# Performance work log

Hardware: AMD Instinct MI355X
Metric: run time of the kernel (lower is better)

Reference implementation:

```python
import jax, jax.numpy as jnp
import numpy as np

# PGA G(3,0,1) blade layout: [1, e0,e1,e2,e3, e01,e02,e03,e12,e13,e23, e012,e013,e023,e123, e0123]
GRADE = jnp.array([0, 1, 1, 1, 1, 2, 2, 2, 2, 2, 2, 3, 3, 3, 3, 4])
# invariant inner product uses only blades not containing the degenerate e0
INNER_IDX = jnp.array([0, 2, 3, 4, 8, 9, 10, 14])

B, N, IN_MV, IN_S = 1, 1024, 16, 128
H, HID_MV, HID_S = 8, 4, 32
C_Z, OUT_MV, OUT_S = 128, 16, 128
ROPE_BASE = 4096.0


def equi_linear(mv, w5):
    # grade-wise equivariant channel mixing: w5 [out, in, 5] -> per-blade weight [out, in, 16]
    w16 = w5[:, :, GRADE]
    return jnp.einsum('...ib,oib->...ob', mv, w16)


def rope(x, base=ROPE_BASE):
    # rotary positional encoding along item axis 1; last dim must be even
    n, d = x.shape[1], x.shape[-1]
    half = d // 2
    freqs = base ** (-jnp.arange(half, dtype=x.dtype) / half)
    ang = jnp.arange(n, dtype=x.dtype)[:, None] * freqs  # [N, half]
    shp = (1, n) + (1,) * (x.ndim - 3) + (half,)
    cos, sin = jnp.cos(ang).reshape(shp), jnp.sin(ang).reshape(shp)
    x1, x2 = x[..., 0::2], x[..., 1::2]
    return jnp.stack([x1 * cos - x2 * sin, x1 * sin + x2 * cos], axis=-1).reshape(x.shape)


def setup_inputs() -> dict:
    key = jax.random.key(0)
    ks = jax.random.split(key, 16)
    sc_mv = 1.0 / np.sqrt(IN_MV)
    sc_s = 1.0 / np.sqrt(IN_S)
    return {
        'mv': jax.random.normal(ks[0], (B, N, IN_MV, 16), jnp.float32),
        's': jax.random.normal(ks[1], (B, N, IN_S), jnp.float32),
        'z': jax.random.normal(ks[2], (B, N, N, C_Z), jnp.float32),
        'q_w_mv': jax.random.normal(ks[3], (H * HID_MV, IN_MV, 5), jnp.float32) * sc_mv,
        'q_w_s': jax.random.normal(ks[4], (H * HID_S, IN_S), jnp.float32) * sc_s,
        'k_w_mv': jax.random.normal(ks[5], (HID_MV, IN_MV, 5), jnp.float32) * sc_mv,
        'k_w_s': jax.random.normal(ks[6], (HID_S, IN_S), jnp.float32) * sc_s,
        'v_w_mv': jax.random.normal(ks[7], (HID_MV, IN_MV, 5), jnp.float32) * sc_mv,
        'v_w_s': jax.random.normal(ks[8], (HID_S, IN_S), jnp.float32) * sc_s,
        'out_w_mv': jax.random.normal(ks[9], (OUT_MV, H * HID_MV, 5), jnp.float32) / np.sqrt(H * HID_MV),
        'out_w_s': jax.random.normal(ks[10], (OUT_S, H * HID_S), jnp.float32) / np.sqrt(H * HID_S),
        'ln_g': jnp.ones((C_Z,), jnp.float32),
        'ln_b': jnp.zeros((C_Z,), jnp.float32),
        'bias_w': jax.random.normal(ks[11], (C_Z, H), jnp.float32) / np.sqrt(C_Z),
    }


def reference(mv, s, z, q_w_mv, q_w_s, k_w_mv, k_w_s, v_w_mv, v_w_s,
              out_w_mv, out_w_s, ln_g, ln_b, bias_w):
    b, n = mv.shape[0], mv.shape[1]
    # multi-query QKV: queries per-head, shared single-head K/V
    q_mv = equi_linear(mv, q_w_mv).reshape(b, n, H, HID_MV, 16)
    q_s = jnp.einsum('bns,os->bno', s, q_w_s).reshape(b, n, H, HID_S)
    k_mv = equi_linear(mv, k_w_mv)                     # [B,N,hid_mv,16]
    k_s = jnp.einsum('bns,os->bno', s, k_w_s)          # [B,N,hid_s]
    v_mv = equi_linear(mv, v_w_mv)
    v_s = jnp.einsum('bns,os->bno', s, v_w_s)
    # rotary encoding on scalar queries/keys
    q_s, k_s = rope(q_s), rope(k_s)
    # invariant attention features: non-degenerate mv components + scalars
    qf = jnp.concatenate([q_mv[..., INNER_IDX].reshape(b, n, H, HID_MV * 8), q_s], axis=-1)
    kf = jnp.concatenate([k_mv[..., INNER_IDX].reshape(b, n, HID_MV * 8), k_s], axis=-1)
    d = qf.shape[-1]
    logits = jnp.einsum('bqhd,bkd->bhqk', qf, kf) / jnp.sqrt(jnp.asarray(d, qf.dtype))
    # pair bias: Linear(LayerNorm(z)) -> heads
    mu = jnp.mean(z, axis=-1, keepdims=True)
    var = jnp.var(z, axis=-1, keepdims=True)
    zn = (z - mu) * jax.lax.rsqrt(var + 1e-5) * ln_g + ln_b
    bias = jnp.einsum('bqkc,ch->bhqk', zn, bias_w)
    attn = jax.nn.softmax(logits + bias, axis=-1)      # [B,H,N,N]
    o_mv = jnp.einsum('bhqk,bkcx->bqhcx', attn, v_mv).reshape(b, n, H * HID_MV, 16)
    o_s = jnp.einsum('bhqk,bkc->bqhc', attn, v_s).reshape(b, n, H * HID_S)
    out_mv = equi_linear(o_mv, out_w_mv)               # [B,N,out_mv,16]
    out_s = jnp.einsum('bnc,oc->bno', o_s, out_w_s)    # [B,N,out_s]
    return out_mv, out_s
```

## Files before the change

kernel.cpp:

```cpp
#include <hip/hip_runtime.h>
#include <hip/hip_bf16.h>

__device__ __constant__ int GRADE_C[16] = {0,1,1,1,1,2,2,2,2,2,2,3,3,3,3,4};
__device__ __constant__ int INNER_C[8]  = {0,2,3,4,8,9,10,14};

#define OFF_GH    0
#define GWBT_BYTE 4096
#define KFB_BYTE  16384
#define VTB_BYTE  262144
#define QFB_BYTE  524288
#define SB_BYTE   3145728

typedef __attribute__((ext_vector_type(8))) short bf16x8;
typedef __attribute__((ext_vector_type(4))) float f32x4;
typedef __attribute__((ext_vector_type(4))) unsigned int u32x4;

static __device__ __forceinline__ unsigned short f2bf(float f) {
    unsigned int u = __float_as_uint(f);
    u = u + 0x7fffu + ((u >> 16) & 1u);
    return (unsigned short)(u >> 16);
}
static __device__ __forceinline__ unsigned pk2(float lo, float hi) {
    return (unsigned)f2bf(lo) | ((unsigned)f2bf(hi) << 16);
}
static __device__ __forceinline__ unsigned cvtpk(float lo, float hi) {
    __hip_bfloat162 c = __float22bfloat162_rn(make_float2(lo, hi));
    unsigned u;
    __builtin_memcpy(&u, &c, 4);
    return u;
}
static __device__ __forceinline__ float bflo(unsigned int u) {
    return __uint_as_float(u << 16);
}
static __device__ __forceinline__ float bfhi(unsigned int u) {
    return __uint_as_float(u & 0xffff0000u);
}

__global__ __launch_bounds__(256) void kproj(
    const float* __restrict__ mv, const float* __restrict__ s,
    const float* __restrict__ q_w_mv, const float* __restrict__ q_w_s,
    const float* __restrict__ k_w_mv, const float* __restrict__ k_w_s,
    const float* __restrict__ v_w_mv, const float* __restrict__ v_w_s,
    const float* __restrict__ ln_g, const float* __restrict__ ln_b,
    const float* __restrict__ bias_w, float* __restrict__ ws)
{
    __shared__ __align__(16) float mvn[256];
    __shared__ __align__(16) float sn[128];
    __shared__ float qs_pre[256];
    __shared__ float ks_pre[32];
    __shared__ float vs_pre[32];
    const int n = blockIdx.x, t = threadIdx.x;

    unsigned short* kfb = (unsigned short*)((char*)ws + KFB_BYTE);
    unsigned short* qfb = (unsigned short*)((char*)ws + QFB_BYTE);
    unsigned short* gwp = (unsigned short*)((char*)ws + GWBT_BYTE);
    unsigned short* vtb = (unsigned short*)((char*)ws + VTB_BYTE);

    mvn[t] = mv[n * 256 + t];
    if (t < 128) sn[t] = s[n * 128 + t];
    __syncthreads();

    {
        const float4* w = (const float4*)(q_w_s + t * 128);
        const float4* sv = (const float4*)sn;
        float acc = 0.f;
        #pragma unroll
        for (int c4 = 0; c4 < 32; ++c4) {
            float4 wv = w[c4], x = sv[c4];
            acc += wv.x * x.x + wv.y * x.y + wv.z * x.z + wv.w * x.w;
        }
        qs_pre[t] = acc;
    }
    if (t < 64) {
        const float* wb = (t < 32) ? (k_w_s + t * 128) : (v_w_s + (t - 32) * 128);
        const float4* w = (const float4*)wb;
        const float4* sv = (const float4*)sn;
        float acc = 0.f;
        #pragma unroll
        for (int c4 = 0; c4 < 32; ++c4) {
            float4 wv = w[c4], x = sv[c4];
            acc += wv.x * x.x + wv.y * x.y + wv.z * x.z + wv.w * x.w;
        }
        if (t < 32) ks_pre[t] = acc; else vs_pre[t - 32] = acc;
    }
    {
        int o = t >> 3, j = t & 7;
        int bx = INNER_C[j], g = GRADE_C[bx];
        float acc = 0.f;
        #pragma unroll
        for (int i = 0; i < 16; ++i)
            acc += mvn[i * 16 + bx] * q_w_mv[(o * 16 + i) * 5 + g];
        int h = o >> 2, c = o & 3, d = c * 8 + j;
        qfb[n * 1024 + h * 64 + d] = f2bf(acc);
    }
    {
        int hp = 8 + (t >> 5), d = t & 31;
        qfb[n * 1024 + hp * 64 + d] = 0;
        qfb[n * 1024 + hp * 64 + 32 + d] = 0;
    }
    if (t < 32) {
        int bx = INNER_C[t & 7], g = GRADE_C[bx];
        float acc = 0.f;
        #pragma unroll
        for (int i = 0; i < 16; ++i)
            acc += mvn[i * 16 + bx] * k_w_mv[((t >> 3) * 16 + i) * 5 + g];
        kfb[n * 64 + t] = f2bf(acc);
    }
    if (t >= 64 && t < 128) {
        int idx = t - 64, x = idx & 15, g = GRADE_C[x];
        float acc = 0.f;
        #pragma unroll
        for (int i = 0; i < 16; ++i)
            acc += mvn[i * 16 + x] * v_w_mv[((idx >> 4) * 16 + i) * 5 + g];
        vtb[idx * 1024 + n] = f2bf(acc);
    }
    __syncthreads();

    {
        int h = t >> 5, dd = t & 31, i = dd >> 1;
        float freq = exp2f(-0.75f * (float)i);
        float ang = (float)n * freq;
        float cv = cosf(ang), sv = sinf(ang);
        float x1 = qs_pre[h * 32 + 2 * i], x2 = qs_pre[h * 32 + 2 * i + 1];
        float val = ((dd & 1) == 0) ? (x1 * cv - x2 * sv) : (x1 * sv + x2 * cv);
        qfb[n * 1024 + h * 64 + 32 + dd] = f2bf(val);
    }
    if (t < 32) {
        int i = t >> 1;
        float freq = exp2f(-0.75f * (float)i);
        float ang = (float)n * freq;
        float cv = cosf(ang), sv = sinf(ang);
        float x1 = ks_pre[2 * i], x2 = ks_pre[2 * i + 1];
        float val = ((t & 1) == 0) ? (x1 * cv - x2 * sv) : (x1 * sv + x2 * cv);
        kfb[n * 64 + 32 + t] = f2bf(val);
    }
    if (t >= 32 && t < 64) vtb[(64 + t - 32) * 1024 + n] = f2bf(vs_pre[t - 32]);

    if (n == 0) {
        if (t < 128) {
            int cb = t >> 5, r = t & 31;
            int lg, e;
            if (r < 16) { lg = r >> 2; e = r & 3; }
            else        { lg = (r - 16) >> 2; e = 4 + (r & 3); }
            int pos = cb * 32 + lg * 8 + e;
            float g = ln_g[t];
            #pragma unroll
            for (int j = 0; j < 8; ++j)
                gwp[j * 128 + pos] = f2bf(g * bias_w[t * 8 + j]);
            gwp[8 * 128 + pos] = 0x3F80;
            #pragma unroll
            for (int j = 9; j < 16; ++j) gwp[j * 128 + pos] = 0;
        }
        if (t >= 128 && t < 136) {
            int h = t - 128;
            float gh = 0.f, ch = 0.f;
            for (int c = 0; c < 128; ++c) {
                gh += ln_g[c] * bias_w[c * 8 + h];
                ch += ln_b[c] * bias_w[c * 8 + h];
            }
            ws[OFF_GH + h] = gh;
            ws[OFF_GH + 8 + h] = ch;
        }
    }
}

__global__ __launch_bounds__(256, 4) void kbias(
    const float* __restrict__ z, float* __restrict__ ws)
{
    __shared__ float d1[128][17];
    __shared__ float d2[128][17];
    __shared__ float ssq[128];
    const int blk = blockIdx.x;
    const int q = blk >> 3, kblk = blk & 7;
    const int t = threadIdx.x, w = t >> 6, l = t & 63;
    const int lm = l & 15, lg = l >> 4;

    bf16x8 B1[4], B2[2];
    #pragma unroll
    for (int ks = 0; ks < 4; ++ks)
        B1[ks] = *(const bf16x8*)((const char*)ws + GWBT_BYTE + (lm * 128 + ks * 32 + lg * 8) * 2);
    #pragma unroll
    for (int ds = 0; ds < 2; ++ds)
        B2[ds] = *(const bf16x8*)((const char*)ws + QFB_BYTE + ((size_t)q * 1024 + lm * 64 + ds * 32 + lg * 8) * 2);

    float4 za[2][4], zb[2][4];
    #pragma unroll
    for (int mi = 0; mi < 2; ++mi) {
        const int krow = kblk * 128 + (w * 2 + mi) * 16 + lm;
        const float* zr = z + ((size_t)q * 1024 + krow) * 128 + lg * 4;
        #pragma unroll
        for (int ks = 0; ks < 4; ++ks) {
            za[mi][ks] = *(const float4*)(zr + ks * 32);
            zb[mi][ks] = *(const float4*)(zr + ks * 32 + 16);
        }
    }

    #pragma unroll
    for (int mi = 0; mi < 2; ++mi) {
        const int mt = w * 2 + mi;
        const int krow = kblk * 128 + mt * 16 + lm;
        bf16x8 A2[2];
        #pragma unroll
        for (int ds = 0; ds < 2; ++ds)
            A2[ds] = *(const bf16x8*)((const char*)ws + KFB_BYTE + ((size_t)krow * 64 + ds * 32 + lg * 8) * 2);

        f32x4 acc1 = {0.f, 0.f, 0.f, 0.f};
        f32x4 acc2 = {0.f, 0.f, 0.f, 0.f};
        float sq = 0.f;
        #pragma unroll
        for (int ks = 0; ks < 4; ++ks) {
            float4 A = za[mi][ks], Bv = zb[mi][ks];
            sq = __builtin_fmaf(A.x, A.x, sq);  sq = __builtin_fmaf(A.y, A.y, sq);
            sq = __builtin_fmaf(A.z, A.z, sq);  sq = __builtin_fmaf(A.w, A.w, sq);
            sq = __builtin_fmaf(Bv.x, Bv.x, sq); sq = __builtin_fmaf(Bv.y, Bv.y, sq);
            sq = __builtin_fmaf(Bv.z, Bv.z, sq); sq = __builtin_fmaf(Bv.w, Bv.w, sq);
            u32x4 au;
            au[0] = cvtpk(A.x, A.y);   au[1] = cvtpk(A.z, A.w);
            au[2] = cvtpk(Bv.x, Bv.y); au[3] = cvtpk(Bv.z, Bv.w);
            bf16x8 af = __builtin_bit_cast(bf16x8, au);
            acc1 = __builtin_amdgcn_mfma_f32_16x16x32_bf16(af, B1[ks], acc1, 0, 0, 0);
        }
        acc2 = __builtin_amdgcn_mfma_f32_16x16x32_bf16(A2[0], B2[0], acc2, 0, 0, 0);
        acc2 = __builtin_amdgcn_mfma_f32_16x16x32_bf16(A2[1], B2[1], acc2, 0, 0, 0);

        sq += __shfl_xor(sq, 16);
        sq += __shfl_xor(sq, 32);
        if (lg == 0) ssq[mt * 16 + lm] = sq;

        #pragma unroll
        for (int r = 0; r < 4; ++r) {
            int row = mt * 16 + lg * 4 + r;
            d1[row][lm] = acc1[r];
            d2[row][lm] = acc2[r];
        }
    }
    __syncthreads();

    {
        const int r = t >> 1, hb = t & 1;
        float sum = d1[r][8];
        float sq = ssq[r];
        float mean = sum * (1.f / 128.f);
        float var = sq * (1.f / 128.f) - mean * mean;
        float rs = rsqrtf(var + 1e-5f);
        unsigned short u[4];
        #pragma unroll
        for (int j = 0; j < 4; ++j) {
            int h = hb * 4 + j;
            float bias = rs * (d1[r][h] - mean * ws[OFF_GH + h]) + ws[OFF_GH + 8 + h];
            u[j] = f2bf(d2[r][h] * 0.125f + bias);
        }
        uint2 pk;
        pk.x = (unsigned)u[0] | ((unsigned)u[1] << 16);
        pk.y = (unsigned)u[2] | ((unsigned)u[3] << 16);
        unsigned short* sb = (unsigned short*)((char*)ws + SB_BYTE);
        *(uint2*)(sb + ((size_t)q * 1024 + kblk * 128 + r) * 8 + hb * 4) = pk;
    }
}

__global__ __launch_bounds__(512) void kattn(
    const float* __restrict__ ws,
    const float* __restrict__ out_w_mv, const float* __restrict__ out_w_s,
    float* __restrict__ d_out)
{
    __shared__ __align__(16) unsigned int Pb[16 * 512];
    __shared__ float inv_l[8];
    __shared__ float o_sh[8 * 96];
    const int q = blockIdx.x, t = threadIdx.x;

    const unsigned short* sb =
        (const unsigned short*)((const char*)ws + SB_BYTE) + (size_t)q * 8192;
    {
        int wd = t;
        uint4 r0 = *(const uint4*)(sb + (size_t)wd * 16);
        uint4 r1 = *(const uint4*)(sb + (size_t)wd * 16 + 8);
        Pb[0 * 512 + (wd ^ (0 << 2))] = (r0.x & 0xffffu) | (r1.x << 16);
        Pb[1 * 512 + (wd ^ (1 << 2))] = (r0.x >> 16) | (r1.x & 0xffff0000u);
        Pb[2 * 512 + (wd ^ (2 << 2))] = (r0.y & 0xffffu) | (r1.y << 16);
        Pb[3 * 512 + (wd ^ (3 << 2))] = (r0.y >> 16) | (r1.y & 0xffff0000u);
        Pb[4 * 512 + (wd ^ (4 << 2))] = (r0.z & 0xffffu) | (r1.z << 16);
        Pb[5 * 512 + (wd ^ (5 << 2))] = (r0.z >> 16) | (r1.z & 0xffff0000u);
        Pb[6 * 512 + (wd ^ (6 << 2))] = (r0.w & 0xffffu) | (r1.w << 16);
        Pb[7 * 512 + (wd ^ (7 << 2))] = (r0.w >> 16) | (r1.w & 0xffff0000u);
    }
    __syncthreads();

    const int h = t >> 6, e = t & 63;
    const int hx = (h & 7) << 2;
    unsigned int* Ph = &Pb[h * 512];
    float m = -1e30f;
    #pragma unroll
    for (int j = 0; j < 8; ++j) {
        unsigned int v = Ph[(e + j * 64) ^ hx];
        m = fmaxf(m, fmaxf(bflo(v), bfhi(v)));
    }
    #pragma unroll
    for (int d = 32; d >= 1; d >>= 1) m = fmaxf(m, __shfl_xor(m, d));
    float lsum = 0.f;
    #pragma unroll
    for (int j = 0; j < 8; ++j) {
        int idx = (e + j * 64) ^ hx;
        unsigned int v = Ph[idx];
        float p0 = __expf(bflo(v) - m);
        float p1 = __expf(bfhi(v) - m);
        lsum += p0 + p1;
        Ph[idx] = pk2(p0, p1);
    }
    #pragma unroll
    for (int d = 32; d >= 1; d >>= 1) lsum += __shfl_xor(lsum, d);
    if (e == 0) inv_l[h] = 1.f / lsum;
    __syncthreads();

    const int wv = t >> 6, l = t & 63, lm = l & 15, lg = l >> 4;
    const unsigned short* vtb = (const unsigned short*)((const char*)ws + VTB_BYTE);
    const char* PbB = (const char*)Pb;
    if (wv < 6) {
        int mt = wv;
        f32x4 acc = {0.f, 0.f, 0.f, 0.f};
        #pragma unroll 8
        for (int ks = 0; ks < 32; ++ks) {
            bf16x8 a = *(const bf16x8*)(vtb + (size_t)(mt * 16 + lm) * 1024 + ks * 32 + lg * 8);
            bf16x8 b = *(const bf16x8*)(PbB + lm * 2048 + ((ks * 64 + lg * 16) ^ ((lm & 7) << 4)));
            acc = __builtin_amdgcn_mfma_f32_16x16x32_bf16(a, b, acc, 0, 0, 0);
        }
        if (lm < 8) {
            float il = inv_l[lm];
            #pragma unroll
            for (int r = 0; r < 4; ++r)
                o_sh[lm * 96 + mt * 16 + lg * 4 + r] = acc[r] * il;
        }
    }
    __syncthreads();

    if (t < 256) {
        int o2 = t >> 4, b = t & 15, g = GRADE_C[b];
        float acc = 0.f;
        #pragma unroll
        for (int i = 0; i < 32; ++i)
            acc += o_sh[(i >> 2) * 96 + (i & 3) * 16 + b] *
                   out_w_mv[(o2 * 32 + i) * 5 + g];
        d_out[(q * 16 + o2) * 16 + b] = acc;
    }
    if (t >= 256 && t < 384) {
        int tt = t - 256;
        const float* wv2 = out_w_s + tt * 256;
        float acc = 0.f;
        #pragma unroll 4
        for (int c = 0; c < 256; ++c)
            acc += o_sh[(c >> 5) * 96 + 64 + (c & 31)] * wv2[c];
        d_out[262144 + q * 128 + tt] = acc;
    }
}

extern "C" void kernel_launch(void* const* d_in, const int* in_sizes, int n_in,
                              void* d_out, int out_size, void* d_ws, size_t ws_size,
                              hipStream_t stream) {
    (void)in_sizes; (void)n_in; (void)out_size; (void)ws_size;
    const float* mv       = (const float*)d_in[0];
    const float* s        = (const float*)d_in[1];
    const float* z        = (const float*)d_in[2];
    const float* q_w_mv   = (const float*)d_in[3];
    const float* q_w_s    = (const float*)d_in[4];
    const float* k_w_mv   = (const float*)d_in[5];
    const float* k_w_s    = (const float*)d_in[6];
    const float* v_w_mv   = (const float*)d_in[7];
    const float* v_w_s    = (const float*)d_in[8];
    const float* out_w_mv = (const float*)d_in[9];
    const float* out_w_s  = (const float*)d_in[10];
    const float* ln_g     = (const float*)d_in[11];
    const float* ln_b     = (const float*)d_in[12];
    const float* bias_w   = (const float*)d_in[13];
    float* ws  = (float*)d_ws;
    float* out = (float*)d_out;

    kproj<<<1024, 256, 0, stream>>>(mv, s, q_w_mv, q_w_s, k_w_mv, k_w_s,
                                    v_w_mv, v_w_s, ln_g, ln_b, bias_w, ws);
    kbias<<<8192, 256, 0, stream>>>(z, ws);
    kattn<<<1024, 512, 0, stream>>>(ws, out_w_mv, out_w_s, out);
}
```

Before: 186.9 us.

## Fuse pair-bias and attention kernels into one per-query kernel

Merges the bias kernel (8192 blocks) and the attention kernel into a single kernel with one block per query. The block loops over eight key blocks, keeping the bf16 logits in shared memory instead of writing them to and reading them back from a workspace buffer. Finalisation of each key block is software-pipelined so it runs alongside the next block's z loads. This drops one launch and the logits round trip through global memory, but parallelism falls to 1024 blocks with a serial loop over keys. Occupancy may drop and the z stream could become latency-bound.

```diff
diff --git a/kernel.cpp b/kernel.cpp
--- a/kernel.cpp
+++ b/kernel.cpp
@@ -9,7 +9,6 @@
 #define KFB_BYTE  16384
 #define VTB_BYTE  262144
 #define QFB_BYTE  524288
-#define SB_BYTE   3145728
 
 typedef __attribute__((ext_vector_type(8))) short bf16x8;
 typedef __attribute__((ext_vector_type(4))) float f32x4;
@@ -35,6 +34,11 @@
 static __device__ __forceinline__ float bfhi(unsigned int u) {
     return __uint_as_float(u & 0xffff0000u);
 }
+
+#define LDS_BAR() do { \
+    asm volatile("s_waitcnt lgkmcnt(0)" ::: "memory"); \
+    __builtin_amdgcn_s_barrier(); \
+} while (0)
 
 __global__ __launch_bounds__(256) void kproj(
     const float* __restrict__ mv, const float* __restrict__ s,
@@ -164,16 +168,23 @@
     }
 }
 
-__global__ __launch_bounds__(256, 4) void kbias(
-    const float* __restrict__ z, float* __restrict__ ws)
+__global__ __launch_bounds__(256, 3) void kfused(
+    const float* __restrict__ z, const float* __restrict__ ws,
+    const float* __restrict__ out_w_mv, const float* __restrict__ out_w_s,
+    float* __restrict__ d_out)
 {
     __shared__ float d1[128][17];
     __shared__ float d2[128][17];
     __shared__ float ssq[128];
-    const int blk = blockIdx.x;
-    const int q = blk >> 3, kblk = blk & 7;
-    const int t = threadIdx.x, w = t >> 6, l = t & 63;
-    const int lm = l & 15, lg = l >> 4;
+    __shared__ float GhCh_s[16];
+    __shared__ __align__(16) unsigned int Pb[8 * 512];
+    __shared__ float inv_l[8];
+    __shared__ float o_sh[8 * 96];
+
+    const int q = blockIdx.x, t = threadIdx.x;
+    const int w = t >> 6, l = t & 63, lm = l & 15, lg = l >> 4;
+
+    if (t < 16) GhCh_s[t] = ws[OFF_GH + t];
 
     bf16x8 B1[4], B2[2];
     #pragma unroll
@@ -183,156 +194,157 @@
     for (int ds = 0; ds < 2; ++ds)
         B2[ds] = *(const bf16x8*)((const char*)ws + QFB_BYTE + ((size_t)q * 1024 + lm * 64 + ds * 32 + lg * 8) * 2);
 
-    float4 za[2][4], zb[2][4];
-    #pragma unroll
-    for (int mi = 0; mi < 2; ++mi) {
-        const int krow = kblk * 128 + (w * 2 + mi) * 16 + lm;
-        const float* zr = z + ((size_t)q * 1024 + krow) * 128 + lg * 4;
-        #pragma unroll
-        for (int ks = 0; ks < 4; ++ks) {
-            za[mi][ks] = *(const float4*)(zr + ks * 32);
-            zb[mi][ks] = *(const float4*)(zr + ks * 32 + 16);
-        }
-    }
-
-    #pragma unroll
-    for (int mi = 0; mi < 2; ++mi) {
-        const int mt = w * 2 + mi;
-        const int krow = kblk * 128 + mt * 16 + lm;
-        bf16x8 A2[2];
-        #pragma unroll
-        for (int ds = 0; ds < 2; ++ds)
-            A2[ds] = *(const bf16x8*)((const char*)ws + KFB_BYTE + ((size_t)krow * 64 + ds * 32 + lg * 8) * 2);
-
-        f32x4 acc1 = {0.f, 0.f, 0.f, 0.f};
-        f32x4 acc2 = {0.f, 0.f, 0.f, 0.f};
-        float sq = 0.f;
-        #pragma unroll
-        for (int ks = 0; ks < 4; ++ks) {
-            float4 A = za[mi][ks], Bv = zb[mi][ks];
-            sq = __builtin_fmaf(A.x, A.x, sq);  sq = __builtin_fmaf(A.y, A.y, sq);
-            sq = __builtin_fmaf(A.z, A.z, sq);  sq = __builtin_fmaf(A.w, A.w, sq);
-            sq = __builtin_fmaf(Bv.x, Bv.x, sq); sq = __builtin_fmaf(Bv.y, Bv.y, sq);
-            sq = __builtin_fmaf(Bv.z, Bv.z, sq); sq = __builtin_fmaf(Bv.w, Bv.w, sq);
-            u32x4 au;
-            au[0] = cvtpk(A.x, A.y);   au[1] = cvtpk(A.z, A.w);
-            au[2] = cvtpk(Bv.x, Bv.y); au[3] = cvtpk(Bv.z, Bv.w);
-            bf16x8 af = __builtin_bit_cast(bf16x8, au);
-            acc1 = __builtin_amdgcn_mfma_f32_16x16x32_bf16(af, B1[ks], acc1, 0, 0, 0);
-        }
-        acc2 = __builtin_amdgcn_mfma_f32_16x16x32_bf16(A2[0], B2[0], acc2, 0, 0, 0);
-        acc2 = __builtin_amdgcn_mfma_f32_16x16x32_bf16(A2[1], B2[1], acc2, 0, 0, 0);
-
-        sq += __shfl_xor(sq, 16);
-        sq += __shfl_xor(sq, 32);
-        if (lg == 0) ssq[mt * 16 + lm] = sq;
-
-        #pragma unroll
-        for (int r = 0; r < 4; ++r) {
-            int row = mt * 16 + lg * 4 + r;
-            d1[row][lm] = acc1[r];
-            d2[row][lm] = acc2[r];
-        }
-    }
-    __syncthreads();
-
-    {
-        const int r = t >> 1, hb = t & 1;
-        float sum = d1[r][8];
-        float sq = ssq[r];
-        float mean = sum * (1.f / 128.f);
-        float var = sq * (1.f / 128.f) - mean * mean;
-        float rs = rsqrtf(var + 1e-5f);
-        unsigned short u[4];
+    const unsigned short* kfb = (const unsigned short*)((const char*)ws + KFB_BYTE);
+
+    for (int kb = 0; kb < 8; ++kb) {
+        float4 za[2][4], zb[2][4];
+        bf16x8 A2[2][2];
+        #pragma unroll
+        for (int mi = 0; mi < 2; ++mi) {
+            const int krow = kb * 128 + (w * 2 + mi) * 16 + lm;
+            const float* zr = z + ((size_t)q * 1024 + krow) * 128 + lg * 4;
+            #pragma unroll
+            for (int ks = 0; ks < 4; ++ks) {
+                za[mi][ks] = *(const float4*)(zr + ks * 32);
+                zb[mi][ks] = *(const float4*)(zr + ks * 32 + 16);
+            }
+            #pragma unroll
+            for (int ds = 0; ds < 2; ++ds)
+                A2[mi][ds] = *(const bf16x8*)(kfb + (size_t)krow * 64 + ds * 32 + lg * 8);
+        }
+
+        if (kb > 0 && t < 128) {
+            const int p = t >> 1, hg = t & 1;
+            const int rr0 = 2 * p, rr1 = rr0 + 1;
+            float mean0 = d1[rr0][8] * (1.f / 128.f);
+            float var0  = ssq[rr0] * (1.f / 128.f) - mean0 * mean0;
+            float rs0   = rsqrtf(var0 + 1e-5f);
+            float mean1 = d1[rr1][8] * (1.f / 128.f);
+            float var1  = ssq[rr1] * (1.f / 128.f) - mean1 * mean1;
+            float rs1   = rsqrtf(var1 + 1e-5f);
+            const int wbase = (kb - 1) * 64 + p;
+            #pragma unroll
+            for (int j = 0; j < 4; ++j) {
+                int h = hg * 4 + j;
+                float b0 = rs0 * (d1[rr0][h] - mean0 * GhCh_s[h]) + GhCh_s[8 + h];
+                float s0 = d2[rr0][h] * 0.125f + b0;
+                float b1 = rs1 * (d1[rr1][h] - mean1 * GhCh_s[h]) + GhCh_s[8 + h];
+                float s1 = d2[rr1][h] * 0.125f + b1;
+                Pb[h * 512 + (wbase ^ (h << 2))] = pk2(s0, s1);
+            }
+        }
+        LDS_BAR();
+
+        #pragma unroll
+        for (int mi = 0; mi < 2; ++mi) {
+            const int mt = w * 2 + mi;
+            f32x4 acc1 = {0.f, 0.f, 0.f, 0.f};
+            f32x4 acc2 = {0.f, 0.f, 0.f, 0.f};
+            float sq = 0.f;
+            #pragma unroll
+            for (int ks = 0; ks < 4; ++ks) {
+                float4 A = za[mi][ks], Bv = zb[mi][ks];
+                sq = __builtin_fmaf(A.x, A.x, sq);   sq = __builtin_fmaf(A.y, A.y, sq);
+                sq = __builtin_fmaf(A.z, A.z, sq);   sq = __builtin_fmaf(A.w, A.w, sq);
+                sq = __builtin_fmaf(Bv.x, Bv.x, sq); sq = __builtin_fmaf(Bv.y, Bv.y, sq);
+                sq = __builtin_fmaf(Bv.z, Bv.z, sq); sq = __builtin_fmaf(Bv.w, Bv.w, sq);
+                u32x4 au;
+                au[0] = cvtpk(A.x, A.y);   au[1] = cvtpk(A.z, A.w);
+                au[2] = cvtpk(Bv.x, Bv.y); au[3] = cvtpk(Bv.z, Bv.w);
+                bf16x8 af = __builtin_bit_cast(bf16x8, au);
+                acc1 = __builtin_amdgcn_mfma_f32_16x16x32_bf16(af, B1[ks], acc1, 0, 0, 0);
+            }
+            acc2 = __builtin_amdgcn_mfma_f32_16x16x32_bf16(A2[mi][0], B2[0], acc2, 0, 0, 0);
+            acc2 = __builtin_amdgcn_mfma_f32_16x16x32_bf16(A2[mi][1], B2[1], acc2, 0, 0, 0);
+
+            sq += __shfl_xor(sq, 16);
+            sq += __shfl_xor(sq, 32);
+            if (lg == 0) ssq[mt * 16 + lm] = sq;
+
+            #pragma unroll
+            for (int r = 0; r < 4; ++r) {
+                int row = mt * 16 + lg * 4 + r;
+                d1[row][lm] = acc1[r];
+                d2[row][lm] = acc2[r];
+            }
+        }
+        LDS_BAR();
+    }
+
+    if (t < 128) {
+        const int p = t >> 1, hg = t & 1;
+        const int rr0 = 2 * p, rr1 = rr0 + 1;
+        float mean0 = d1[rr0][8] * (1.f / 128.f);
+        float var0  = ssq[rr0] * (1.f / 128.f) - mean0 * mean0;
+        float rs0   = rsqrtf(var0 + 1e-5f);
+        float mean1 = d1[rr1][8] * (1.f / 128.f);
+        float var1  = ssq[rr1] * (1.f / 128.f) - mean1 * mean1;
+        float rs1   = rsqrtf(var1 + 1e-5f);
+        const int wbase = 7 * 64 + p;
         #pragma unroll
         for (int j = 0; j < 4; ++j) {
-            int h = hb * 4 + j;
-            float bias = rs * (d1[r][h] - mean * ws[OFF_GH + h]) + ws[OFF_GH + 8 + h];
-            u[j] = f2bf(d2[r][h] * 0.125f + bias);
-        }
-        uint2 pk;
-        pk.x = (unsigned)u[0] | ((unsigned)u[1] << 16);
-        pk.y = (unsigned)u[2] | ((unsigned)u[3] << 16);
-        unsigned short* sb = (unsigned short*)((char*)ws + SB_BYTE);
-        *(uint2*)(sb + ((size_t)q * 1024 + kblk * 128 + r) * 8 + hb * 4) = pk;
-    }
-}
-
-__global__ __launch_bounds__(512) void kattn(
-    const float* __restrict__ ws,
-    const float* __restrict__ out_w_mv, const float* __restrict__ out_w_s,
-    float* __restrict__ d_out)
-{
-    __shared__ __align__(16) unsigned int Pb[16 * 512];
-    __shared__ float inv_l[8];
-    __shared__ float o_sh[8 * 96];
-    const int q = blockIdx.x, t = threadIdx.x;
-
-    const unsigned short* sb =
-        (const unsigned short*)((const char*)ws + SB_BYTE) + (size_t)q * 8192;
-    {
-        int wd = t;
-        uint4 r0 = *(const uint4*)(sb + (size_t)wd * 16);
-        uint4 r1 = *(const uint4*)(sb + (size_t)wd * 16 + 8);
-        Pb[0 * 512 + (wd ^ (0 << 2))] = (r0.x & 0xffffu) | (r1.x << 16);
-        Pb[1 * 512 + (wd ^ (1 << 2))] = (r0.x >> 16) | (r1.x & 0xffff0000u);
-        Pb[2 * 512 + (wd ^ (2 << 2))] = (r0.y & 0xffffu) | (r1.y << 16);
-        Pb[3 * 512 + (wd ^ (3 << 2))] = (r0.y >> 16) | (r1.y & 0xffff0000u);
-        Pb[4 * 512 + (wd ^ (4 << 2))] = (r0.z & 0xffffu) | (r1.z << 16);
-        Pb[5 * 512 + (wd ^ (5 << 2))] = (r0.z >> 16) | (r1.z & 0xffff0000u);
-        Pb[6 * 512 + (wd ^ (6 << 2))] = (r0.w & 0xffffu) | (r1.w << 16);
-        Pb[7 * 512 + (wd ^ (7 << 2))] = (r0.w >> 16) | (r1.w & 0xffff0000u);
-    }
-    __syncthreads();
-
-    const int h = t >> 6, e = t & 63;
-    const int hx = (h & 7) << 2;
-    unsigned int* Ph = &Pb[h * 512];
-    float m = -1e30f;
-    #pragma unroll
-    for (int j = 0; j < 8; ++j) {
-        unsigned int v = Ph[(e + j * 64) ^ hx];
-        m = fmaxf(m, fmaxf(bflo(v), bfhi(v)));
-    }
-    #pragma unroll
-    for (int d = 32; d >= 1; d >>= 1) m = fmaxf(m, __shfl_xor(m, d));
-    float lsum = 0.f;
-    #pragma unroll
-    for (int j = 0; j < 8; ++j) {
-        int idx = (e + j * 64) ^ hx;
-        unsigned int v = Ph[idx];
-        float p0 = __expf(bflo(v) - m);
-        float p1 = __expf(bfhi(v) - m);
-        lsum += p0 + p1;
-        Ph[idx] = pk2(p0, p1);
-    }
-    #pragma unroll
-    for (int d = 32; d >= 1; d >>= 1) lsum += __shfl_xor(lsum, d);
-    if (e == 0) inv_l[h] = 1.f / lsum;
-    __syncthreads();
-
-    const int wv = t >> 6, l = t & 63, lm = l & 15, lg = l >> 4;
-    const unsigned short* vtb = (const unsigned short*)((const char*)ws + VTB_BYTE);
-    const char* PbB = (const char*)Pb;
-    if (wv < 6) {
-        int mt = wv;
-        f32x4 acc = {0.f, 0.f, 0.f, 0.f};
-        #pragma unroll 8
-        for (int ks = 0; ks < 32; ++ks) {
-            bf16x8 a = *(const bf16x8*)(vtb + (size_t)(mt * 16 + lm) * 1024 + ks * 32 + lg * 8);
-            bf16x8 b = *(const bf16x8*)(PbB + lm * 2048 + ((ks * 64 + lg * 16) ^ ((lm & 7) << 4)));
-            acc = __builtin_amdgcn_mfma_f32_16x16x32_bf16(a, b, acc, 0, 0, 0);
-        }
-        if (lm < 8) {
-            float il = inv_l[lm];
-            #pragma unroll
-            for (int r = 0; r < 4; ++r)
-                o_sh[lm * 96 + mt * 16 + lg * 4 + r] = acc[r] * il;
-        }
-    }
-    __syncthreads();
-
-    if (t < 256) {
+            int h = hg * 4 + j;
+            float b0 = rs0 * (d1[rr0][h] - mean0 * GhCh_s[h]) + GhCh_s[8 + h];
+            float s0 = d2[rr0][h] * 0.125f + b0;
+            float b1 = rs1 * (d1[rr1][h] - mean1 * GhCh_s[h]) + GhCh_s[8 + h];
+            float s1 = d2[rr1][h] * 0.125f + b1;
+            Pb[h * 512 + (wbase ^ (h << 2))] = pk2(s0, s1);
+        }
+    }
+    __syncthreads();
+
+    {
+        const int h = t >> 5, e = t & 31, hx = h << 2;
+        unsigned int* Ph = &Pb[h * 512];
+        float m = -1e30f;
+        #pragma unroll
+        for (int j = 0; j < 16; ++j) {
+            unsigned int v = Ph[(e + j * 32) ^ hx];
+            m = fmaxf(m, fmaxf(bflo(v), bfhi(v)));
+        }
+        #pragma unroll
+        for (int d = 16; d >= 1; d >>= 1) m = fmaxf(m, __shfl_xor(m, d));
+        float lsum = 0.f;
+        #pragma unroll
+        for (int j = 0; j < 16; ++j) {
+            int idx = (e + j * 32) ^ hx;
+            unsigned int v = Ph[idx];
+            float p0 = __expf(bflo(v) - m);
+            float p1 = __expf(bfhi(v) - m);
+            lsum += p0 + p1;
+            Ph[idx] = pk2(p0, p1);
+        }
+        #pragma unroll
+        for (int d = 16; d >= 1; d >>= 1) lsum += __shfl_xor(lsum, d);
+        if (e == 0) inv_l[h] = 1.f / lsum;
+    }
+    __syncthreads();
+
+    {
+        const unsigned short* vtb = (const unsigned short*)((const char*)ws + VTB_BYTE);
+        const char* PbB = (const char*)Pb;
+        const int hh = lm & 7;
+        const int nmt = (w < 2) ? 2 : 1;
+        for (int ii = 0; ii < nmt; ++ii) {
+            int mt = w + ii * 4;
+            f32x4 acc = {0.f, 0.f, 0.f, 0.f};
+            #pragma unroll 8
+            for (int ks = 0; ks < 32; ++ks) {
+                bf16x8 a = *(const bf16x8*)(vtb + (size_t)(mt * 16 + lm) * 1024 + ks * 32 + lg * 8);
+                bf16x8 b = *(const bf16x8*)(PbB + hh * 2048 + ((ks * 64 + lg * 16) ^ (hh << 4)));
+                acc = __builtin_amdgcn_mfma_f32_16x16x32_bf16(a, b, acc, 0, 0, 0);
+            }
+            if (lm < 8) {
+                float il = inv_l[lm];
+                #pragma unroll
+                for (int r = 0; r < 4; ++r)
+                    o_sh[lm * 96 + mt * 16 + lg * 4 + r] = acc[r] * il;
+            }
+        }
+    }
+    __syncthreads();
+
+    {
         int o2 = t >> 4, b = t & 15, g = GRADE_C[b];
         float acc = 0.f;
         #pragma unroll
@@ -341,14 +353,13 @@
                    out_w_mv[(o2 * 32 + i) * 5 + g];
         d_out[(q * 16 + o2) * 16 + b] = acc;
     }
-    if (t >= 256 && t < 384) {
-        int tt = t - 256;
-        const float* wv2 = out_w_s + tt * 256;
+    if (t < 128) {
+        const float* wv2 = out_w_s + t * 256;
         float acc = 0.f;
         #pragma unroll 4
         for (int c = 0; c < 256; ++c)
             acc += o_sh[(c >> 5) * 96 + 64 + (c & 31)] * wv2[c];
-        d_out[262144 + q * 128 + tt] = acc;
+        d_out[262144 + q * 128 + t] = acc;
     }
 }
 
@@ -375,6 +386,5 @@
 
     kproj<<<1024, 256, 0, stream>>>(mv, s, q_w_mv, q_w_s, k_w_mv, k_w_s,
                                     v_w_mv, v_w_s, ln_g, ln_b, bias_w, ws);
-    kbias<<<8192, 256, 0, stream>>>(z, ws);
-    kattn<<<1024, 512, 0, stream>>>(ws, out_w_mv, out_w_s, out);
-}
+    kfused<<<1024, 256, 0, stream>>>(z, ws, out_w_mv, out_w_s, out);
+}
```

Measured after the change: 178.1 us. -4.7%, faster.

## Fuse pair-bias and attention kernels with double-buffered LDS staging of z

Applied to the files above, without the earlier changes.

Merges the bias kernel and the attention kernel into one per-query kernel. The per-row bias logits stay in LDS instead of being written to and re-read from a global scratch buffer, and one launch is removed. z rows are streamed into a 128KB double-buffered LDS ring with async global_load_lds, using swizzled addressing and explicit vmcnt waits so that loads overlap MFMA work. In exchange, the 144KB LDS footprint limits occupancy to one block per CU, the grid shrinks from 8192 to 1024 blocks, and each block now performs the full z pass serially over eight stages.

```diff
diff --git a/kernel.cpp b/kernel.cpp
--- a/kernel.cpp
+++ b/kernel.cpp
@@ -9,7 +9,6 @@
 #define KFB_BYTE  16384
 #define VTB_BYTE  262144
 #define QFB_BYTE  524288
-#define SB_BYTE   3145728
 
 typedef __attribute__((ext_vector_type(8))) short bf16x8;
 typedef __attribute__((ext_vector_type(4))) float f32x4;
@@ -34,6 +33,12 @@
 }
 static __device__ __forceinline__ float bfhi(unsigned int u) {
     return __uint_as_float(u & 0xffff0000u);
+}
+
+static __device__ __forceinline__ void gload16(const void* g, void* l) {
+    __builtin_amdgcn_global_load_lds(
+        (const __attribute__((address_space(1))) unsigned int*)g,
+        (__attribute__((address_space(3))) unsigned int*)l, 16, 0, 0);
 }
 
 __global__ __launch_bounds__(256) void kproj(
@@ -164,54 +169,78 @@
     }
 }
 
-__global__ __launch_bounds__(256, 4) void kbias(
-    const float* __restrict__ z, float* __restrict__ ws)
+__global__ __launch_bounds__(512) void kfused(
+    const float* __restrict__ z, const float* __restrict__ ws,
+    const float* __restrict__ out_w_mv, const float* __restrict__ out_w_s,
+    float* __restrict__ d_out)
 {
-    __shared__ float d1[128][17];
-    __shared__ float d2[128][17];
-    __shared__ float ssq[128];
-    const int blk = blockIdx.x;
-    const int q = blk >> 3, kblk = blk & 7;
-    const int t = threadIdx.x, w = t >> 6, l = t & 63;
-    const int lm = l & 15, lg = l >> 4;
-
-    bf16x8 B1[4], B2[2];
+    __shared__ __align__(16) char lds[147456];
+    unsigned int* Pb = (unsigned int*)(lds + 131072);
+    float* o_sh  = (float*)lds;
+    float* inv_l = (float*)(lds + 3072);
+
+    const int q = blockIdx.x, t = threadIdx.x;
+    const int w = t >> 6, l = t & 63, lm = l & 15, lg = l >> 4;
+
+    bf16x8 B1[4], B2[2], A2[8][2];
     #pragma unroll
     for (int ks = 0; ks < 4; ++ks)
         B1[ks] = *(const bf16x8*)((const char*)ws + GWBT_BYTE + (lm * 128 + ks * 32 + lg * 8) * 2);
     #pragma unroll
     for (int ds = 0; ds < 2; ++ds)
         B2[ds] = *(const bf16x8*)((const char*)ws + QFB_BYTE + ((size_t)q * 1024 + lm * 64 + ds * 32 + lg * 8) * 2);
-
-    float4 za[2][4], zb[2][4];
+    {
+        const unsigned short* kfb = (const unsigned short*)((const char*)ws + KFB_BYTE);
+        #pragma unroll
+        for (int p = 0; p < 8; ++p) {
+            int krow = p * 128 + w * 16 + lm;
+            A2[p][0] = *(const bf16x8*)(kfb + (size_t)krow * 64 + lg * 8);
+            A2[p][1] = *(const bf16x8*)(kfb + (size_t)krow * 64 + 32 + lg * 8);
+        }
+    }
+    const float Gh_l = ws[OFF_GH + (lm & 7)];
+    const float Ch_l = ws[OFF_GH + 8 + (lm & 7)];
+
+    const char* zq = (const char*)z + (size_t)q * 1024 * 512;
+    const int srow = l >> 5, schunk = l & 31;
+
+#define STAGE(p, b) do {                                                        \
+    const char* zp_ = zq + ((size_t)(p) * 128 + w * 16) * 512;                  \
+    char* lb_ = lds + (b) * 65536 + w * 8192;                                   \
+    _Pragma("unroll")                                                           \
+    for (int i_ = 0; i_ < 8; ++i_) {                                            \
+        int R_ = i_ * 2 + srow;                                                 \
+        gload16(zp_ + (size_t)R_ * 512 + ((schunk ^ R_) << 4), lb_ + i_ * 1024);\
+    }                                                                           \
+} while (0)
+
+    asm volatile("s_waitcnt vmcnt(0)" ::: "memory");
+    STAGE(0, 0);
+    STAGE(1, 1);
+
     #pragma unroll
-    for (int mi = 0; mi < 2; ++mi) {
-        const int krow = kblk * 128 + (w * 2 + mi) * 16 + lm;
-        const float* zr = z + ((size_t)q * 1024 + krow) * 128 + lg * 4;
+    for (int p = 0; p < 8; ++p) {
+        if (p < 7) { asm volatile("s_waitcnt vmcnt(8)" ::: "memory"); }
+        else       { asm volatile("s_waitcnt vmcnt(0)" ::: "memory"); }
+        __builtin_amdgcn_sched_barrier(0);
+        __builtin_amdgcn_s_barrier();
+
+        const char* zt = lds + (p & 1) * 65536 + (w * 16 + lm) * 512;
+        float4 za[4], zb4[4];
         #pragma unroll
         for (int ks = 0; ks < 4; ++ks) {
-            za[mi][ks] = *(const float4*)(zr + ks * 32);
-            zb[mi][ks] = *(const float4*)(zr + ks * 32 + 16);
-        }
-    }
-
-    #pragma unroll
-    for (int mi = 0; mi < 2; ++mi) {
-        const int mt = w * 2 + mi;
-        const int krow = kblk * 128 + mt * 16 + lm;
-        bf16x8 A2[2];
-        #pragma unroll
-        for (int ds = 0; ds < 2; ++ds)
-            A2[ds] = *(const bf16x8*)((const char*)ws + KFB_BYTE + ((size_t)krow * 64 + ds * 32 + lg * 8) * 2);
+            za[ks]  = *(const float4*)(zt + (((lg + ks * 8)     ^ lm) << 4));
+            zb4[ks] = *(const float4*)(zt + (((lg + ks * 8 + 4) ^ lm) << 4));
+        }
 
         f32x4 acc1 = {0.f, 0.f, 0.f, 0.f};
         f32x4 acc2 = {0.f, 0.f, 0.f, 0.f};
         float sq = 0.f;
         #pragma unroll
         for (int ks = 0; ks < 4; ++ks) {
-            float4 A = za[mi][ks], Bv = zb[mi][ks];
-            sq = __builtin_fmaf(A.x, A.x, sq);  sq = __builtin_fmaf(A.y, A.y, sq);
-            sq = __builtin_fmaf(A.z, A.z, sq);  sq = __builtin_fmaf(A.w, A.w, sq);
+            float4 A = za[ks], Bv = zb4[ks];
+            sq = __builtin_fmaf(A.x, A.x, sq);   sq = __builtin_fmaf(A.y, A.y, sq);
+            sq = __builtin_fmaf(A.z, A.z, sq);   sq = __builtin_fmaf(A.w, A.w, sq);
             sq = __builtin_fmaf(Bv.x, Bv.x, sq); sq = __builtin_fmaf(Bv.y, Bv.y, sq);
             sq = __builtin_fmaf(Bv.z, Bv.z, sq); sq = __builtin_fmaf(Bv.w, Bv.w, sq);
             u32x4 au;
@@ -220,114 +249,80 @@
             bf16x8 af = __builtin_bit_cast(bf16x8, au);
             acc1 = __builtin_amdgcn_mfma_f32_16x16x32_bf16(af, B1[ks], acc1, 0, 0, 0);
         }
-        acc2 = __builtin_amdgcn_mfma_f32_16x16x32_bf16(A2[0], B2[0], acc2, 0, 0, 0);
-        acc2 = __builtin_amdgcn_mfma_f32_16x16x32_bf16(A2[1], B2[1], acc2, 0, 0, 0);
+        acc2 = __builtin_amdgcn_mfma_f32_16x16x32_bf16(A2[p][0], B2[0], acc2, 0, 0, 0);
+        acc2 = __builtin_amdgcn_mfma_f32_16x16x32_bf16(A2[p][1], B2[1], acc2, 0, 0, 0);
 
         sq += __shfl_xor(sq, 16);
         sq += __shfl_xor(sq, 32);
-        if (lg == 0) ssq[mt * 16 + lm] = sq;
-
+
+        float sval[4];
         #pragma unroll
         for (int r = 0; r < 4; ++r) {
-            int row = mt * 16 + lg * 4 + r;
-            d1[row][lm] = acc1[r];
-            d2[row][lm] = acc2[r];
-        }
-    }
-    __syncthreads();
-
-    {
-        const int r = t >> 1, hb = t & 1;
-        float sum = d1[r][8];
-        float sq = ssq[r];
-        float mean = sum * (1.f / 128.f);
-        float var = sq * (1.f / 128.f) - mean * mean;
-        float rs = rsqrtf(var + 1e-5f);
-        unsigned short u[4];
-        #pragma unroll
-        for (int j = 0; j < 4; ++j) {
-            int h = hb * 4 + j;
-            float bias = rs * (d1[r][h] - mean * ws[OFF_GH + h]) + ws[OFF_GH + 8 + h];
-            u[j] = f2bf(d2[r][h] * 0.125f + bias);
-        }
-        uint2 pk;
-        pk.x = (unsigned)u[0] | ((unsigned)u[1] << 16);
-        pk.y = (unsigned)u[2] | ((unsigned)u[3] << 16);
-        unsigned short* sb = (unsigned short*)((char*)ws + SB_BYTE);
-        *(uint2*)(sb + ((size_t)q * 1024 + kblk * 128 + r) * 8 + hb * 4) = pk;
-    }
-}
-
-__global__ __launch_bounds__(512) void kattn(
-    const float* __restrict__ ws,
-    const float* __restrict__ out_w_mv, const float* __restrict__ out_w_s,
-    float* __restrict__ d_out)
-{
-    __shared__ __align__(16) unsigned int Pb[16 * 512];
-    __shared__ float inv_l[8];
-    __shared__ float o_sh[8 * 96];
-    const int q = blockIdx.x, t = threadIdx.x;
-
-    const unsigned short* sb =
-        (const unsigned short*)((const char*)ws + SB_BYTE) + (size_t)q * 8192;
-    {
-        int wd = t;
-        uint4 r0 = *(const uint4*)(sb + (size_t)wd * 16);
-        uint4 r1 = *(const uint4*)(sb + (size_t)wd * 16 + 8);
-        Pb[0 * 512 + (wd ^ (0 << 2))] = (r0.x & 0xffffu) | (r1.x << 16);
-        Pb[1 * 512 + (wd ^ (1 << 2))] = (r0.x >> 16) | (r1.x & 0xffff0000u);
-        Pb[2 * 512 + (wd ^ (2 << 2))] = (r0.y & 0xffffu) | (r1.y << 16);
-        Pb[3 * 512 + (wd ^ (3 << 2))] = (r0.y >> 16) | (r1.y & 0xffff0000u);
-        Pb[4 * 512 + (wd ^ (4 << 2))] = (r0.z & 0xffffu) | (r1.z << 16);
-        Pb[5 * 512 + (wd ^ (5 << 2))] = (r0.z >> 16) | (r1.z & 0xffff0000u);
-        Pb[6 * 512 + (wd ^ (6 << 2))] = (r0.w & 0xffffu) | (r1.w << 16);
-        Pb[7 * 512 + (wd ^ (7 << 2))] = (r0.w >> 16) | (r1.w & 0xffff0000u);
-    }
-    __syncthreads();
-
-    const int h = t >> 6, e = t & 63;
-    const int hx = (h & 7) << 2;
-    unsigned int* Ph = &Pb[h * 512];
-    float m = -1e30f;
-    #pragma unroll
-    for (int j = 0; j < 8; ++j) {
-        unsigned int v = Ph[(e + j * 64) ^ hx];
-        m = fmaxf(m, fmaxf(bflo(v), bfhi(v)));
-    }
-    #pragma unroll
-    for (int d = 32; d >= 1; d >>= 1) m = fmaxf(m, __shfl_xor(m, d));
-    float lsum = 0.f;
-    #pragma unroll
-    for (int j = 0; j < 8; ++j) {
-        int idx = (e + j * 64) ^ hx;
-        unsigned int v = Ph[idx];
-        float p0 = __expf(bflo(v) - m);
-        float p1 = __expf(bfhi(v) - m);
-        lsum += p0 + p1;
-        Ph[idx] = pk2(p0, p1);
-    }
-    #pragma unroll
-    for (int d = 32; d >= 1; d >>= 1) lsum += __shfl_xor(lsum, d);
-    if (e == 0) inv_l[h] = 1.f / lsum;
-    __syncthreads();
-
-    const int wv = t >> 6, l = t & 63, lm = l & 15, lg = l >> 4;
-    const unsigned short* vtb = (const unsigned short*)((const char*)ws + VTB_BYTE);
-    const char* PbB = (const char*)Pb;
-    if (wv < 6) {
-        int mt = wv;
-        f32x4 acc = {0.f, 0.f, 0.f, 0.f};
-        #pragma unroll 8
-        for (int ks = 0; ks < 32; ++ks) {
-            bf16x8 a = *(const bf16x8*)(vtb + (size_t)(mt * 16 + lm) * 1024 + ks * 32 + lg * 8);
-            bf16x8 b = *(const bf16x8*)(PbB + lm * 2048 + ((ks * 64 + lg * 16) ^ ((lm & 7) << 4)));
-            acc = __builtin_amdgcn_mfma_f32_16x16x32_bf16(a, b, acc, 0, 0, 0);
+            float ssq_r = __shfl(sq, lg * 4 + r);
+            float sum_r = __shfl(acc1[r], lg * 16 + 8);
+            float mean = sum_r * (1.f / 128.f);
+            float var  = ssq_r * (1.f / 128.f) - mean * mean;
+            float rs   = rsqrtf(var + 1e-5f);
+            float bias = rs * (acc1[r] - mean * Gh_l) + Ch_l;
+            sval[r] = acc2[r] * 0.125f + bias;
         }
         if (lm < 8) {
-            float il = inv_l[lm];
-            #pragma unroll
-            for (int r = 0; r < 4; ++r)
-                o_sh[lm * 96 + mt * 16 + lg * 4 + r] = acc[r] * il;
+            int wp = p * 64 + w * 8 + lg * 2;
+            Pb[lm * 512 + ( wp      ^ (lm << 2))] = cvtpk(sval[0], sval[1]);
+            Pb[lm * 512 + ((wp + 1) ^ (lm << 2))] = cvtpk(sval[2], sval[3]);
+        }
+
+        __builtin_amdgcn_s_barrier();
+        if (p < 6) STAGE(p + 2, p & 1);
+    }
+    __syncthreads();
+
+    {
+        const int h = t >> 6, e = t & 63, hx = h << 2;
+        unsigned int* Ph = &Pb[h * 512];
+        float m = -1e30f;
+        #pragma unroll
+        for (int j = 0; j < 8; ++j) {
+            unsigned int v = Ph[(e + j * 64) ^ hx];
+            m = fmaxf(m, fmaxf(bflo(v), bfhi(v)));
+        }
+        #pragma unroll
+        for (int d = 32; d >= 1; d >>= 1) m = fmaxf(m, __shfl_xor(m, d));
+        float lsum = 0.f;
+        #pragma unroll
+        for (int j = 0; j < 8; ++j) {
+            int idx = (e + j * 64) ^ hx;
+            unsigned int v = Ph[idx];
+            float p0 = __expf(bflo(v) - m);
+            float p1 = __expf(bfhi(v) - m);
+            lsum += p0 + p1;
+            Ph[idx] = pk2(p0, p1);
+        }
+        #pragma unroll
+        for (int d = 32; d >= 1; d >>= 1) lsum += __shfl_xor(lsum, d);
+        if (e == 0) inv_l[h] = 1.f / lsum;
+    }
+    __syncthreads();
+
+    {
+        const unsigned short* vtb = (const unsigned short*)((const char*)ws + VTB_BYTE);
+        const char* PbB = (const char*)Pb;
+        const int hh = lm & 7;
+        if (w < 6) {
+            int mt = w;
+            f32x4 acc = {0.f, 0.f, 0.f, 0.f};
+            #pragma unroll 8
+            for (int ks = 0; ks < 32; ++ks) {
+                bf16x8 a = *(const bf16x8*)(vtb + (size_t)(mt * 16 + lm) * 1024 + ks * 32 + lg * 8);
+                bf16x8 b = *(const bf16x8*)(PbB + hh * 2048 + ((ks * 64 + lg * 16) ^ (hh << 4)));
+                acc = __builtin_amdgcn_mfma_f32_16x16x32_bf16(a, b, acc, 0, 0, 0);
+            }
+            if (lm < 8) {
+                float il = inv_l[lm];
+                #pragma unroll
+                for (int r = 0; r < 4; ++r)
+                    o_sh[lm * 96 + mt * 16 + lg * 4 + r] = acc[r] * il;
+            }
         }
     }
     __syncthreads();
@@ -350,6 +345,7 @@
             acc += o_sh[(c >> 5) * 96 + 64 + (c & 31)] * wv2[c];
         d_out[262144 + q * 128 + tt] = acc;
     }
+#undef STAGE
 }
 
 extern "C" void kernel_launch(void* const* d_in, const int* in_sizes, int n_in,
@@ -375,6 +371,5 @@
 
     kproj<<<1024, 256, 0, stream>>>(mv, s, q_w_mv, q_w_s, k_w_mv, k_w_s,
                                     v_w_mv, v_w_s, ln_g, ln_b, bias_w, ws);
-    kbias<<<8192, 256, 0, stream>>>(z, ws);
-    kattn<<<1024, 512, 0, stream>>>(ws, out_w_mv, out_w_s, out);
-}
+    kfused<<<1024, 512, 0, stream>>>(z, ws, out_w_mv, out_w_s, out);
+}
```

Result: slower. 197.6 us (+5.7%).
